# Performance work log

Measured on AMD Instinct MI355X. Metric: run time of the kernel, lower is better.

## Reference

```python
import jax, jax.numpy as jnp
import numpy as np


def _box_filter(img):
    # img: [B,1,H,W]; 5x5 uniform kernel, padding=4 -> output [B,1,H+4,W+4]
    k = jnp.full((1, 1, 5, 5), 1.0 / 25.0, dtype=img.dtype)
    return jax.lax.conv_general_dilated(
        img, k, window_strides=(1, 1), padding=((4, 4), (4, 4)),
        dimension_numbers=('NCHW', 'OIHW', 'NCHW'))


def setup_inputs() -> dict:
    key = jax.random.key(0)
    k1, k2 = jax.random.split(key)
    x = jax.random.normal(k1, (64, 1, 512, 512), dtype=jnp.float32)
    y = jax.random.normal(k2, (64, 1, 512, 512), dtype=jnp.float32)
    return {"x": x, "y": y}


def reference(x, y):
    diff = _box_filter(x) - _box_filter(y)
    # faithful to torch.mean(torch.sqrt(diff * diff)) (== mean(|diff|))
    return jnp.mean(jnp.sqrt(diff * diff))
```

## Files before the change

kernel.cpp:

```cpp
#include <hip/hip_runtime.h>


#define TR      12
#define STRIPS  43
#define NWAVES  (64 * STRIPS)
#define NBLOCKS (NWAVES / 4)

__global__ __launch_bounds__(256) void box_loss_kernel(
    const float* __restrict__ x, const float* __restrict__ y,
    float* __restrict__ ws, float* __restrict__ out)
{
    __shared__ float wsum[4];

    const int lane  = threadIdx.x & 63;
    const int wid   = (blockIdx.x << 2) + (threadIdx.x >> 6);
    const int img   = wid / STRIPS;
    const int strip = wid - img * STRIPS;
    const int i0    = strip * TR;

    const size_t base = (size_t)img * (512 * 512) + (size_t)(lane * 8);
    const float* xb = x + base;
    const float* yb = y + base;

    float hist[5][8];
    float v[8];
    #pragma unroll
    for (int j = 0; j < 8; ++j) v[j] = 0.f;
    #pragma unroll
    for (int s = 0; s < 5; ++s)
        #pragma unroll
        for (int j = 0; j < 8; ++j) hist[s][j] = 0.f;

    float acc = 0.f;

    #pragma unroll
    for (int k = 0; k < TR + 4; ++k) {
        const int r  = i0 - 4 + k;
        const int rc = min(max(r, 0), 511);
        const bool valid = (r == rc);
        const float* xr = xb + (size_t)rc * 512;
        const float* yr = yb + (size_t)rc * 512;
        float4 xa = ((const float4*)xr)[0];
        float4 xc = ((const float4*)xr)[1];
        float4 ya = ((const float4*)yr)[0];
        float4 yc = ((const float4*)yr)[1];

        float d[8];
        d[0] = xa.x - ya.x; d[1] = xa.y - ya.y; d[2] = xa.z - ya.z; d[3] = xa.w - ya.w;
        d[4] = xc.x - yc.x; d[5] = xc.y - yc.y; d[6] = xc.z - yc.z; d[7] = xc.w - yc.w;
        #pragma unroll
        for (int j = 0; j < 8; ++j) d[j] = valid ? d[j] : 0.f;

        const int slot = k % 5;
        #pragma unroll
        for (int j = 0; j < 8; ++j) {
            v[j] += d[j] - hist[slot][j];
            hist[slot][j] = d[j];
        }

        if (k >= 4) {
            float h0 = __shfl_up(v[4], 1, 64);
            float h1 = __shfl_up(v[5], 1, 64);
            float h2 = __shfl_up(v[6], 1, 64);
            float h3 = __shfl_up(v[7], 1, 64);
            if (lane == 0) { h0 = 0.f; h1 = 0.f; h2 = 0.f; h3 = 0.f; }

            float s = h0 + h1 + h2 + h3 + v[0];
            acc += fabsf(s);
            s += v[1] - h0;  acc += fabsf(s);
            s += v[2] - h1;  acc += fabsf(s);
            s += v[3] - h2;  acc += fabsf(s);
            s += v[4] - h3;  acc += fabsf(s);
            s += v[5] - v[0]; acc += fabsf(s);
            s += v[6] - v[1]; acc += fabsf(s);
            s += v[7] - v[2]; acc += fabsf(s);
            if (lane == 63) {
                float t = v[7];  acc += fabsf(t);
                t += v[6];       acc += fabsf(t);
                t += v[5];       acc += fabsf(t);
                t += v[4];       acc += fabsf(t);
            }
        }
    }

    #pragma unroll
    for (int off = 32; off > 0; off >>= 1)
        acc += __shfl_down(acc, off, 64);
    if (lane == 0) wsum[threadIdx.x >> 6] = acc;
    __syncthreads();

    if (threadIdx.x == 0) {
        float s = wsum[0] + wsum[1] + wsum[2] + wsum[3];
        atomicAdd(ws, s);
        __threadfence();
        unsigned* cnt = (unsigned*)(ws + 1);
        unsigned done = atomicAdd(cnt, 1u);
        if (done == (unsigned)(gridDim.x - 1)) {
            float total = atomicAdd(ws, 0.0f);
            out[0] = total * (1.0f / (25.0f * 64.0f * 516.0f * 516.0f));
        }
    }
}

extern "C" void kernel_launch(void* const* d_in, const int* in_sizes, int n_in,
                              void* d_out, int out_size, void* d_ws, size_t ws_size,
                              hipStream_t stream) {
    const float* x = (const float*)d_in[0];
    const float* y = (const float*)d_in[1];
    float* out = (float*)d_out;
    float* ws  = (float*)d_ws;

    hipMemsetAsync(ws, 0, 8, stream);

    box_loss_kernel<<<NBLOCKS, 256, 0, stream>>>(x, y, ws, out);
}
```

Baseline: 172.4 us.

## Shrink strips to 4 rows and issue all row loads up front

```diff
diff --git a/kernel.cpp b/kernel.cpp
--- a/kernel.cpp
+++ b/kernel.cpp
@@ -1,10 +1,9 @@
 #include <hip/hip_runtime.h>
 
 
-#define TR      12
-#define STRIPS  43
-#define NWAVES  (64 * STRIPS)
-#define NBLOCKS (NWAVES / 4)
+#define TR      4
+#define STRIPS  129
+#define NBLOCKS ((STRIPS * 64) / 4)
 
 __global__ __launch_bounds__(256) void box_loss_kernel(
     const float* __restrict__ x, const float* __restrict__ y,
@@ -22,64 +21,66 @@
     const float* xb = x + base;
     const float* yb = y + base;
 
-    float hist[5][8];
+    float4 xs[8][2], ys[8][2];
+    #pragma unroll
+    for (int k = 0; k < 8; ++k) {
+        const int r  = i0 - 4 + k;
+        const int rc = min(max(r, 0), 511);
+        const float4* xr = (const float4*)(xb + (size_t)rc * 512);
+        const float4* yr = (const float4*)(yb + (size_t)rc * 512);
+        xs[k][0] = xr[0]; xs[k][1] = xr[1];
+        ys[k][0] = yr[0]; ys[k][1] = yr[1];
+    }
+
+    float d[8][8];
+    #pragma unroll
+    for (int k = 0; k < 8; ++k) {
+        const int r = i0 - 4 + k;
+        const bool valid = (r >= 0) & (r < 512);
+        d[k][0] = xs[k][0].x - ys[k][0].x;
+        d[k][1] = xs[k][0].y - ys[k][0].y;
+        d[k][2] = xs[k][0].z - ys[k][0].z;
+        d[k][3] = xs[k][0].w - ys[k][0].w;
+        d[k][4] = xs[k][1].x - ys[k][1].x;
+        d[k][5] = xs[k][1].y - ys[k][1].y;
+        d[k][6] = xs[k][1].z - ys[k][1].z;
+        d[k][7] = xs[k][1].w - ys[k][1].w;
+        #pragma unroll
+        for (int j = 0; j < 8; ++j) d[k][j] = valid ? d[k][j] : 0.f;
+    }
+
+    float acc = 0.f;
     float v[8];
     #pragma unroll
-    for (int j = 0; j < 8; ++j) v[j] = 0.f;
-    #pragma unroll
-    for (int s = 0; s < 5; ++s)
-        #pragma unroll
-        for (int j = 0; j < 8; ++j) hist[s][j] = 0.f;
-
-    float acc = 0.f;
+    for (int j = 0; j < 8; ++j)
+        v[j] = d[0][j] + d[1][j] + d[2][j] + d[3][j] + d[4][j];
 
     #pragma unroll
-    for (int k = 0; k < TR + 4; ++k) {
-        const int r  = i0 - 4 + k;
-        const int rc = min(max(r, 0), 511);
-        const bool valid = (r == rc);
-        const float* xr = xb + (size_t)rc * 512;
-        const float* yr = yb + (size_t)rc * 512;
-        float4 xa = ((const float4*)xr)[0];
-        float4 xc = ((const float4*)xr)[1];
-        float4 ya = ((const float4*)yr)[0];
-        float4 yc = ((const float4*)yr)[1];
+    for (int t = 0; t < TR; ++t) {
+        if (t > 0) {
+            #pragma unroll
+            for (int j = 0; j < 8; ++j) v[j] += d[t + 4][j] - d[t - 1][j];
+        }
+        float h0 = __shfl_up(v[4], 1, 64);
+        float h1 = __shfl_up(v[5], 1, 64);
+        float h2 = __shfl_up(v[6], 1, 64);
+        float h3 = __shfl_up(v[7], 1, 64);
+        if (lane == 0) { h0 = 0.f; h1 = 0.f; h2 = 0.f; h3 = 0.f; }
 
-        float d[8];
-        d[0] = xa.x - ya.x; d[1] = xa.y - ya.y; d[2] = xa.z - ya.z; d[3] = xa.w - ya.w;
-        d[4] = xc.x - yc.x; d[5] = xc.y - yc.y; d[6] = xc.z - yc.z; d[7] = xc.w - yc.w;
-        #pragma unroll
-        for (int j = 0; j < 8; ++j) d[j] = valid ? d[j] : 0.f;
-
-        const int slot = k % 5;
-        #pragma unroll
-        for (int j = 0; j < 8; ++j) {
-            v[j] += d[j] - hist[slot][j];
-            hist[slot][j] = d[j];
-        }
-
-        if (k >= 4) {
-            float h0 = __shfl_up(v[4], 1, 64);
-            float h1 = __shfl_up(v[5], 1, 64);
-            float h2 = __shfl_up(v[6], 1, 64);
-            float h3 = __shfl_up(v[7], 1, 64);
-            if (lane == 0) { h0 = 0.f; h1 = 0.f; h2 = 0.f; h3 = 0.f; }
-
-            float s = h0 + h1 + h2 + h3 + v[0];
-            acc += fabsf(s);
-            s += v[1] - h0;  acc += fabsf(s);
-            s += v[2] - h1;  acc += fabsf(s);
-            s += v[3] - h2;  acc += fabsf(s);
-            s += v[4] - h3;  acc += fabsf(s);
-            s += v[5] - v[0]; acc += fabsf(s);
-            s += v[6] - v[1]; acc += fabsf(s);
-            s += v[7] - v[2]; acc += fabsf(s);
-            if (lane == 63) {
-                float t = v[7];  acc += fabsf(t);
-                t += v[6];       acc += fabsf(t);
-                t += v[5];       acc += fabsf(t);
-                t += v[4];       acc += fabsf(t);
-            }
+        float s = h0 + h1 + h2 + h3 + v[0];
+        acc += fabsf(s);
+        s += v[1] - h0;   acc += fabsf(s);
+        s += v[2] - h1;   acc += fabsf(s);
+        s += v[3] - h2;   acc += fabsf(s);
+        s += v[4] - h3;   acc += fabsf(s);
+        s += v[5] - v[0]; acc += fabsf(s);
+        s += v[6] - v[1]; acc += fabsf(s);
+        s += v[7] - v[2]; acc += fabsf(s);
+        if (lane == 63) {
+            float q = v[7];  acc += fabsf(q);
+            q += v[6];       acc += fabsf(q);
+            q += v[5];       acc += fabsf(q);
+            q += v[4];       acc += fabsf(q);
         }
     }
 
```

Result: slower. 242.2 us (+40.4%).

## Software-pipeline row loads four deep and stagger strip order per image

Applied to the files above, without the earlier changes.

```diff
diff --git a/kernel.cpp b/kernel.cpp
--- a/kernel.cpp
+++ b/kernel.cpp
@@ -3,8 +3,8 @@
 
 #define TR      12
 #define STRIPS  43
-#define NWAVES  (64 * STRIPS)
-#define NBLOCKS (NWAVES / 4)
+#define NBLOCKS ((STRIPS * 64) / 4)
+#define NROWS   (TR + 4)
 
 __global__ __launch_bounds__(256) void box_loss_kernel(
     const float* __restrict__ x, const float* __restrict__ y,
@@ -15,15 +15,28 @@
     const int lane  = threadIdx.x & 63;
     const int wid   = (blockIdx.x << 2) + (threadIdx.x >> 6);
     const int img   = wid / STRIPS;
-    const int strip = wid - img * STRIPS;
+    const int s0    = wid - img * STRIPS;
+    const int strip = (s0 + img * 17) % STRIPS;
     const int i0    = strip * TR;
 
     const size_t base = (size_t)img * (512 * 512) + (size_t)(lane * 8);
     const float* xb = x + base;
     const float* yb = y + base;
 
-    float hist[5][8];
-    float v[8];
+    float4 px[4][2], py[4][2];
+
+    #pragma unroll
+    for (int k = 0; k < 4; ++k) {
+        const int r  = i0 - 4 + k;
+        const int rc = min(max(r, 0), 511);
+        const float4* xr = (const float4*)(xb + (size_t)rc * 512);
+        const float4* yr = (const float4*)(yb + (size_t)rc * 512);
+        px[k][0] = xr[0]; px[k][1] = xr[1];
+        py[k][0] = yr[0]; py[k][1] = yr[1];
+    }
+    __builtin_amdgcn_sched_barrier(0);
+
+    float hist[5][8], v[8];
     #pragma unroll
     for (int j = 0; j < 8; ++j) v[j] = 0.f;
     #pragma unroll
@@ -34,17 +47,23 @@
     float acc = 0.f;
 
     #pragma unroll
-    for (int k = 0; k < TR + 4; ++k) {
-        const int r  = i0 - 4 + k;
-        const int rc = min(max(r, 0), 511);
-        const bool valid = (r == rc);
-        const float* xr = xb + (size_t)rc * 512;
-        const float* yr = yb + (size_t)rc * 512;
-        float4 xa = ((const float4*)xr)[0];
-        float4 xc = ((const float4*)xr)[1];
-        float4 ya = ((const float4*)yr)[0];
-        float4 yc = ((const float4*)yr)[1];
+    for (int k = 0; k < NROWS; ++k) {
+        const int st = k & 3;
+        float4 xa = px[st][0], xc = px[st][1];
+        float4 ya = py[st][0], yc = py[st][1];
 
+        if (k + 4 < NROWS) {
+            const int r  = i0 - 4 + (k + 4);
+            const int rc = min(max(r, 0), 511);
+            const float4* xr = (const float4*)(xb + (size_t)rc * 512);
+            const float4* yr = (const float4*)(yb + (size_t)rc * 512);
+            px[st][0] = xr[0]; px[st][1] = xr[1];
+            py[st][0] = yr[0]; py[st][1] = yr[1];
+        }
+        __builtin_amdgcn_sched_barrier(0);
+
+        const int r = i0 - 4 + k;
+        const bool valid = (r >= 0) & (r < 512);
         float d[8];
         d[0] = xa.x - ya.x; d[1] = xa.y - ya.y; d[2] = xa.z - ya.z; d[3] = xa.w - ya.w;
         d[4] = xc.x - yc.x; d[5] = xc.y - yc.y; d[6] = xc.z - yc.z; d[7] = xc.w - yc.w;
@@ -67,18 +86,18 @@
 
             float s = h0 + h1 + h2 + h3 + v[0];
             acc += fabsf(s);
-            s += v[1] - h0;  acc += fabsf(s);
-            s += v[2] - h1;  acc += fabsf(s);
-            s += v[3] - h2;  acc += fabsf(s);
-            s += v[4] - h3;  acc += fabsf(s);
+            s += v[1] - h0;   acc += fabsf(s);
+            s += v[2] - h1;   acc += fabsf(s);
+            s += v[3] - h2;   acc += fabsf(s);
+            s += v[4] - h3;   acc += fabsf(s);
             s += v[5] - v[0]; acc += fabsf(s);
             s += v[6] - v[1]; acc += fabsf(s);
             s += v[7] - v[2]; acc += fabsf(s);
             if (lane == 63) {
-                float t = v[7];  acc += fabsf(t);
-                t += v[6];       acc += fabsf(t);
-                t += v[5];       acc += fabsf(t);
-                t += v[4];       acc += fabsf(t);
+                float q = v[7];  acc += fabsf(q);
+                q += v[6];       acc += fabsf(q);
+                q += v[5];       acc += fabsf(q);
+                q += v[4];       acc += fabsf(q);
             }
         }
     }
```

New measurement: 178.1 us. +3.3%, slower.
